# Kernel tuning notes

Measured on AMD Instinct MI355X. Metric: run time of the kernel, lower is better.

Reference implementation:

```python
import jax, jax.numpy as jnp
import numpy as np


def setup_inputs() -> dict:
    key0 = jax.random.key(0)
    ks = jax.random.split(key0, 6)
    b, q, k = 4, 256, 1024
    emb_q = emb_k = emb_v = 256
    h = 128
    query = jax.random.normal(ks[0], (b, q, emb_q), dtype=jnp.float32)
    key = jax.random.normal(ks[1], (b, k, emb_k), dtype=jnp.float32)
    value = jax.random.normal(ks[2], (b, k, emb_v), dtype=jnp.float32)
    # linear_uniform_ style init: U(-1/sqrt(in), 1/sqrt(in))
    wq = jax.random.uniform(ks[3], (emb_q, h), minval=-1.0, maxval=1.0) / np.sqrt(emb_q)
    wk = jax.random.uniform(ks[4], (emb_k, h), minval=-1.0, maxval=1.0) / np.sqrt(emb_k)
    wv = jax.random.uniform(ks[5], (h,), minval=-1.0, maxval=1.0) / np.sqrt(h)
    return {"query": query, "key": key, "value": value,
            "weight_query": wq.astype(jnp.float32),
            "weight_key": wk.astype(jnp.float32),
            "weight_value": wv.astype(jnp.float32)}


def reference(query, key, value, weight_query, weight_key, weight_value):
    # Additive (Bahdanau) attention.
    Hq = jnp.einsum('bqe,eh->bqh', query, weight_query)   # (b, q, h)
    Hk = jnp.einsum('bke,eh->bkh', key, weight_key)       # (b, k, h)
    # broadcast-add + tanh: (b, q, k, h)
    H = jnp.tanh(Hq[:, :, None, :] + Hk[:, None, :, :])
    z = jnp.einsum('bqkh,h->bqk', H, weight_value)        # scores (b, q, k)
    a = jax.nn.softmax(z, axis=-1)                        # (b, q, k)
    out = jnp.einsum('bqk,bkv->bqv', a, value)            # (b, q, emb_v)
    return out, a
```

## Files before the change

### kernel.cpp

```cpp
#include <hip/hip_runtime.h>


#define L2E 1.4426950408889634f

__global__ __launch_bounds__(256) void aa_proj_kernel(
    const float* __restrict__ query, const float* __restrict__ key,
    const float* __restrict__ wq, const float* __restrict__ wk,
    float* __restrict__ Eq, float* __restrict__ Ek)
{
    __shared__ float rows_s[16 * 256];
    __shared__ float w_s[64 * 128];
    const int i = blockIdx.x;
    const int t = threadIdx.x;

    const float* src;
    const float* W;
    float* dst;
    if (i < 64) {
        const int r0 = i * 16;
        src = query + r0 * 256; W = wq; dst = Eq + r0 * 128;
    } else {
        const int r0 = (i - 64) * 16;
        src = key + r0 * 256; W = wk; dst = Ek + r0 * 128;
    }

#pragma unroll
    for (int j = 0; j < 4; ++j) {
        const int f = t * 4 + j * 1024;
        *(float4*)&rows_s[f] = *(const float4*)&src[f];
    }

    const int rgr = t >> 5;
    const int hg = t & 31;
    const int ri0 = rgr * 2;
    const int h0 = hg * 4;

    float acc0[4] = {0.f, 0.f, 0.f, 0.f};
    float acc1[4] = {0.f, 0.f, 0.f, 0.f};

    for (int ec = 0; ec < 256; ec += 64) {
        __syncthreads();
#pragma unroll
        for (int j = 0; j < 8; ++j) {
            const int f = t * 4 + j * 1024;
            *(float4*)&w_s[f] = *(const float4*)&W[ec * 128 + f];
        }
        __syncthreads();

        for (int e = 0; e < 64; e += 4) {
            float a0[4], a1[4];
            *(float4*)a0 = *(const float4*)&rows_s[ri0 * 256 + ec + e];
            *(float4*)a1 = *(const float4*)&rows_s[(ri0 + 1) * 256 + ec + e];
#pragma unroll
            for (int j = 0; j < 4; ++j) {
                float w[4];
                *(float4*)w = *(const float4*)&w_s[(e + j) * 128 + h0];
#pragma unroll
                for (int c = 0; c < 4; ++c) {
                    acc0[c] = fmaf(a0[j], w[c], acc0[c]);
                    acc1[c] = fmaf(a1[j], w[c], acc1[c]);
                }
            }
        }
    }

    float o0[4], o1[4];
#pragma unroll
    for (int c = 0; c < 4; ++c) {
        o0[c] = __builtin_amdgcn_exp2f(acc0[c] * (2.0f * L2E));
        o1[c] = __builtin_amdgcn_exp2f(acc1[c] * (2.0f * L2E));
    }
    *(float4*)&dst[ri0 * 128 + h0] = *(float4*)o0;
    *(float4*)&dst[(ri0 + 1) * 128 + h0] = *(float4*)o1;
}

__global__ __launch_bounds__(256) void aa_score_kernel(
    const float* __restrict__ Eq, const float* __restrict__ Ek,
    const float* __restrict__ wv, float* __restrict__ z)
{
    __shared__ float eq_s[16 * 128];
    __shared__ float ek_s[64 * 132];
    __shared__ float wv_s[128];

    const int bid = blockIdx.x;
    const int b = bid >> 8;
    const int qt = (bid >> 4) & 15;
    const int kt = bid & 15;
    const int q0g = b * 256 + qt * 16;
    const int k0g = b * 1024 + kt * 64;
    const int t = threadIdx.x;

    const float* eqsrc = Eq + q0g * 128;
#pragma unroll
    for (int j = 0; j < 2; ++j) {
        const int f = t * 4 + j * 1024;
        *(float4*)&eq_s[f] = *(const float4*)&eqsrc[f];
    }
    const float* eksrc = Ek + k0g * 128;
#pragma unroll
    for (int j = 0; j < 8; ++j) {
        const int f = t * 4 + j * 1024;
        const int ki = f >> 7;
        const int h = f & 127;
        *(float4*)&ek_s[ki * 132 + h] = *(const float4*)&eksrc[f];
    }
    if (t < 128) wv_s[t] = wv[t];
    __syncthreads();

    float wsum = 0.f;
#pragma unroll
    for (int j = 0; j < 32; ++j) {
        float w4[4];
        *(float4*)w4 = *(const float4*)&wv_s[j * 4];
        wsum += (w4[0] + w4[1]) + (w4[2] + w4[3]);
    }

    const int qp = t >> 5;
    const int kp = t & 31;
    const float* eqa = eq_s + (qp * 2) * 128;
    const float* eqb = eqa + 128;
    const float* eka = ek_s + kp * 132;
    const float* ekb = eka + 32 * 132;

    float acc00 = 0.f, acc01 = 0.f, acc10 = 0.f, acc11 = 0.f;

    auto quad = [](const float* x, const float* y, const float* w, float& acc) {
        const float A = fmaf(x[0], y[0], 1.0f);
        const float B = fmaf(x[1], y[1], 1.0f);
        const float C = fmaf(x[2], y[2], 1.0f);
        const float D = fmaf(x[3], y[3], 1.0f);
        const float AB = A * B;
        const float CD = C * D;
        const float n01 = fmaf(w[1], A, w[0] * B);
        const float n23 = fmaf(w[3], C, w[2] * D);
        const float num = fmaf(n01, CD, n23 * AB);
        acc = fmaf(num, __builtin_amdgcn_rcpf(AB * CD), acc);
    };

#pragma unroll 4
    for (int h = 0; h < 128; h += 4) {
        float a0[4], a1[4], b0[4], b1[4], w[4];
        *(float4*)a0 = *(const float4*)(eqa + h);
        *(float4*)a1 = *(const float4*)(eqb + h);
        *(float4*)b0 = *(const float4*)(eka + h);
        *(float4*)b1 = *(const float4*)(ekb + h);
        *(float4*)w  = *(const float4*)(wv_s + h);
        quad(a0, b0, w, acc00);
        quad(a0, b1, w, acc01);
        quad(a1, b0, w, acc10);
        quad(a1, b1, w, acc11);
    }

    const int kl = kt * 64 + kp;
    float* zr0 = z + (size_t)(q0g + qp * 2) * 1024 + kl;
    float* zr1 = zr0 + 1024;
    zr0[0]  = fmaf(-2.f, acc00, wsum);
    zr0[32] = fmaf(-2.f, acc01, wsum);
    zr1[0]  = fmaf(-2.f, acc10, wsum);
    zr1[32] = fmaf(-2.f, acc11, wsum);
}

__global__ __launch_bounds__(256) void aa_softmax_kernel(
    const float* __restrict__ z, float* __restrict__ a)
{
    const int row = blockIdx.x;
    const int t = threadIdx.x;
    const float* zr = z + (size_t)row * 1024;

    float x[4];
    *(float4*)x = *(const float4*)&zr[t * 4];

    float m = fmaxf(fmaxf(x[0], x[1]), fmaxf(x[2], x[3]));
#pragma unroll
    for (int off = 32; off; off >>= 1) m = fmaxf(m, __shfl_xor(m, off));

    __shared__ float redm[4];
    __shared__ float reds[4];
    const int wid = t >> 6;
    if ((t & 63) == 0) redm[wid] = m;
    __syncthreads();
    m = fmaxf(fmaxf(redm[0], redm[1]), fmaxf(redm[2], redm[3]));

    float e[4];
    float s = 0.f;
#pragma unroll
    for (int j = 0; j < 4; ++j) {
        e[j] = __builtin_amdgcn_exp2f((x[j] - m) * L2E);
        s += e[j];
    }
#pragma unroll
    for (int off = 32; off; off >>= 1) s += __shfl_xor(s, off);
    if ((t & 63) == 0) reds[wid] = s;
    __syncthreads();
    s = reds[0] + reds[1] + reds[2] + reds[3];

    const float inv = __builtin_amdgcn_rcpf(s);
    float o[4];
#pragma unroll
    for (int j = 0; j < 4; ++j) o[j] = e[j] * inv;
    *(float4*)&a[(size_t)row * 1024 + t * 4] = *(float4*)o;
}

__global__ __launch_bounds__(256) void aa_pv_partial_kernel(
    const float* __restrict__ a, const float* __restrict__ value,
    float* __restrict__ part)
{
    __shared__ float a_s[16][128];
    __shared__ float red_s[4][4096];
    const int bid = blockIdx.x;
    const int b  = bid >> 7;
    const int qt = (bid >> 3) & 15;
    const int kt = bid & 7;
    const int t = threadIdx.x;

#pragma unroll
    for (int j = 0; j < 2; ++j) {
        const int f = t * 4 + j * 1024;
        const int qs = f >> 7;
        const int k0 = f & 127;
        const float* arow = a + (size_t)(b * 256 + qt * 16 + qs) * 1024 + kt * 128;
        *(float4*)&a_s[qs][k0] = *(const float4*)&arow[k0];
    }
    __syncthreads();

    const int w = t >> 6;
    const int lane = t & 63;
    const int v0 = lane * 4;
    const float* vp = value + (size_t)b * 262144
                    + (size_t)(kt * 128 + w * 32) * 256 + v0;

    float acc[16][4] = {};

#pragma unroll 2
    for (int k4 = 0; k4 < 8; ++k4) {
        float vv[4][4];
#pragma unroll
        for (int r = 0; r < 4; ++r)
            *(float4*)vv[r] = *(const float4*)(vp + (size_t)(k4 * 4 + r) * 256);
#pragma unroll
        for (int q = 0; q < 16; ++q) {
            float aq[4];
            *(float4*)aq = *(const float4*)&a_s[q][w * 32 + k4 * 4];
#pragma unroll
            for (int r = 0; r < 4; ++r)
#pragma unroll
                for (int c = 0; c < 4; ++c)
                    acc[q][c] = fmaf(aq[r], vv[r][c], acc[q][c]);
        }
    }

    float* rs = &red_s[w][v0];
#pragma unroll
    for (int q = 0; q < 16; ++q)
        *(float4*)(rs + q * 256) = *(float4*)acc[q];
    __syncthreads();

    const int g = t >> 6;
    const int l4 = (t & 63) * 4;
    float* po = part + (size_t)bid * 4096;
#pragma unroll
    for (int c = 0; c < 4; ++c) {
        const int i = g * 1024 + c * 256 + l4;
        float s[4];
        *(float4*)s = *(const float4*)&red_s[0][i];
#pragma unroll
        for (int ww = 1; ww < 4; ++ww) {
            float x[4];
            *(float4*)x = *(const float4*)&red_s[ww][i];
            s[0] += x[0]; s[1] += x[1]; s[2] += x[2]; s[3] += x[3];
        }
        *(float4*)(po + i) = *(float4*)s;
    }
}

__global__ __launch_bounds__(256) void aa_pv_reduce_kernel(
    const float* __restrict__ part, float* __restrict__ out)
{
    const int idx = blockIdx.x * 256 + threadIdx.x;
    const int o = idx * 4;
    const int row = o >> 8;
    const int v = o & 255;
    const int b = row >> 8;
    const int q = row & 255;
    const int qt = q >> 4;
    const int qr = q & 15;
    const float* p = part + (size_t)((b * 16 + qt) * 8) * 4096 + qr * 256 + v;

    float s[4] = {0.f, 0.f, 0.f, 0.f};
#pragma unroll
    for (int kt = 0; kt < 8; ++kt) {
        float x[4];
        *(float4*)x = *(const float4*)(p + (size_t)kt * 4096);
        s[0] += x[0]; s[1] += x[1]; s[2] += x[2]; s[3] += x[3];
    }
    *(float4*)&out[o] = *(float4*)s;
}

extern "C" void kernel_launch(void* const* d_in, const int* in_sizes, int n_in,
                              void* d_out, int out_size, void* d_ws, size_t ws_size,
                              hipStream_t stream)
{
    const float* query = (const float*)d_in[0];
    const float* key   = (const float*)d_in[1];
    const float* value = (const float*)d_in[2];
    const float* wq    = (const float*)d_in[3];
    const float* wk    = (const float*)d_in[4];
    const float* wv    = (const float*)d_in[5];

    float* out   = (float*)d_out;
    float* a_out = out + 4 * 256 * 256;

    float* ws = (float*)d_ws;
    float* Eq   = ws;
    float* Ek   = ws + 131072;
    float* z    = ws + 131072 + 524288;
    float* part = ws + 131072 + 524288 + 1048576;

    aa_proj_kernel<<<320, 256, 0, stream>>>(query, key, wq, wk, Eq, Ek);
    aa_score_kernel<<<1024, 256, 0, stream>>>(Eq, Ek, wv, z);
    aa_softmax_kernel<<<1024, 256, 0, stream>>>(z, a_out);
    aa_pv_partial_kernel<<<512, 256, 0, stream>>>(a_out, value, part);
    aa_pv_reduce_kernel<<<256, 256, 0, stream>>>(part, out);
}
```

Baseline: 53.47 us.

## Fuse score computation with row softmax, streaming key projections through LDS

Merges the score and softmax kernels into one. Each 512-thread block owns 4 query rows and streams the batch's 1024 projected keys through shared memory in 128-row chunks, prefetching the next chunk into registers. The full score row stays in registers, so the intermediate z buffer is never written or read back, and one launch disappears. The constant weight-sum term is dropped because softmax is shift-invariant. In exchange, each block re-reads the whole Ek for its batch, giving far more L2 traffic and less register reuse than the old 2x2 tiling, and the grid runs only one large block per CU.

Result: slower. 78.18 us (+46.2%).

```diff
diff --git a/kernel.cpp b/kernel.cpp
--- a/kernel.cpp
+++ b/kernel.cpp
@@ -74,131 +74,105 @@
     *(float4*)&dst[(ri0 + 1) * 128 + h0] = *(float4*)o1;
 }
 
-__global__ __launch_bounds__(256) void aa_score_kernel(
+__global__ __launch_bounds__(512) void aa_score_softmax_kernel(
     const float* __restrict__ Eq, const float* __restrict__ Ek,
-    const float* __restrict__ wv, float* __restrict__ z)
-{
-    __shared__ float eq_s[16 * 128];
-    __shared__ float ek_s[64 * 132];
-    __shared__ float wv_s[128];
+    const float* __restrict__ wv, float* __restrict__ a)
+{
+    __shared__ float ek_s[128 * 132];
 
     const int bid = blockIdx.x;
-    const int b = bid >> 8;
-    const int qt = (bid >> 4) & 15;
-    const int kt = bid & 15;
-    const int q0g = b * 256 + qt * 16;
-    const int k0g = b * 1024 + kt * 64;
-    const int t = threadIdx.x;
-
-    const float* eqsrc = Eq + q0g * 128;
-#pragma unroll
-    for (int j = 0; j < 2; ++j) {
-        const int f = t * 4 + j * 1024;
-        *(float4*)&eq_s[f] = *(const float4*)&eqsrc[f];
-    }
-    const float* eksrc = Ek + k0g * 128;
+    const int b  = bid >> 6;
+    const int qt = bid & 63;
+    const int t  = threadIdx.x;
+    const int qp = t >> 7;
+    const int kc = t & 127;
+    const int q0g = b * 256 + qt * 4;
+
+    const int qrow = __builtin_amdgcn_readfirstlane(q0g + qp);
+    const float* eqp = Eq + (size_t)qrow * 128;
+    const float* ekb = Ek + (size_t)b * 131072;
+
+    float pf[8][4];
 #pragma unroll
     for (int j = 0; j < 8; ++j) {
-        const int f = t * 4 + j * 1024;
-        const int ki = f >> 7;
-        const int h = f & 127;
-        *(float4*)&ek_s[ki * 132 + h] = *(const float4*)&eksrc[f];
-    }
-    if (t < 128) wv_s[t] = wv[t];
-    __syncthreads();
-
-    float wsum = 0.f;
-#pragma unroll
-    for (int j = 0; j < 32; ++j) {
-        float w4[4];
-        *(float4*)w4 = *(const float4*)&wv_s[j * 4];
-        wsum += (w4[0] + w4[1]) + (w4[2] + w4[3]);
-    }
-
-    const int qp = t >> 5;
-    const int kp = t & 31;
-    const float* eqa = eq_s + (qp * 2) * 128;
-    const float* eqb = eqa + 128;
-    const float* eka = ek_s + kp * 132;
-    const float* ekb = eka + 32 * 132;
-
-    float acc00 = 0.f, acc01 = 0.f, acc10 = 0.f, acc11 = 0.f;
-
-    auto quad = [](const float* x, const float* y, const float* w, float& acc) {
-        const float A = fmaf(x[0], y[0], 1.0f);
-        const float B = fmaf(x[1], y[1], 1.0f);
-        const float C = fmaf(x[2], y[2], 1.0f);
-        const float D = fmaf(x[3], y[3], 1.0f);
-        const float AB = A * B;
-        const float CD = C * D;
-        const float n01 = fmaf(w[1], A, w[0] * B);
-        const float n23 = fmaf(w[3], C, w[2] * D);
-        const float num = fmaf(n01, CD, n23 * AB);
-        acc = fmaf(num, __builtin_amdgcn_rcpf(AB * CD), acc);
-    };
-
-#pragma unroll 4
-    for (int h = 0; h < 128; h += 4) {
-        float a0[4], a1[4], b0[4], b1[4], w[4];
-        *(float4*)a0 = *(const float4*)(eqa + h);
-        *(float4*)a1 = *(const float4*)(eqb + h);
-        *(float4*)b0 = *(const float4*)(eka + h);
-        *(float4*)b1 = *(const float4*)(ekb + h);
-        *(float4*)w  = *(const float4*)(wv_s + h);
-        quad(a0, b0, w, acc00);
-        quad(a0, b1, w, acc01);
-        quad(a1, b0, w, acc10);
-        quad(a1, b1, w, acc11);
-    }
-
-    const int kl = kt * 64 + kp;
-    float* zr0 = z + (size_t)(q0g + qp * 2) * 1024 + kl;
-    float* zr1 = zr0 + 1024;
-    zr0[0]  = fmaf(-2.f, acc00, wsum);
-    zr0[32] = fmaf(-2.f, acc01, wsum);
-    zr1[0]  = fmaf(-2.f, acc10, wsum);
-    zr1[32] = fmaf(-2.f, acc11, wsum);
-}
-
-__global__ __launch_bounds__(256) void aa_softmax_kernel(
-    const float* __restrict__ z, float* __restrict__ a)
-{
-    const int row = blockIdx.x;
-    const int t = threadIdx.x;
-    const float* zr = z + (size_t)row * 1024;
-
-    float x[4];
-    *(float4*)x = *(const float4*)&zr[t * 4];
-
-    float m = fmaxf(fmaxf(x[0], x[1]), fmaxf(x[2], x[3]));
+        const int g = t * 4 + j * 2048;
+        *(float4*)pf[j] = *(const float4*)&ekb[g];
+    }
+
+    float zv[8];
+
+#pragma unroll
+    for (int c = 0; c < 8; ++c) {
+#pragma unroll
+        for (int j = 0; j < 8; ++j) {
+            const int g = t * 4 + j * 2048;
+            const int row = g >> 7;
+            const int col = g & 127;
+            *(float4*)&ek_s[row * 132 + col] = *(float4*)pf[j];
+        }
+        __syncthreads();
+
+        if (c < 7) {
+            const float* nx = ekb + (size_t)(c + 1) * 16384;
+#pragma unroll
+            for (int j = 0; j < 8; ++j) {
+                const int g = t * 4 + j * 2048;
+                *(float4*)pf[j] = *(const float4*)&nx[g];
+            }
+        }
+
+        float acc = 0.f;
+        const float* ekr = ek_s + kc * 132;
+#pragma unroll 8
+        for (int h = 0; h < 128; h += 4) {
+            float x[4], w4[4], y[4];
+            *(float4*)x  = *(const float4*)(eqp + h);
+            *(float4*)w4 = *(const float4*)(wv + h);
+            *(float4*)y  = *(const float4*)(ekr + h);
+            const float A = fmaf(x[0], y[0], 1.0f);
+            const float B = fmaf(x[1], y[1], 1.0f);
+            const float C = fmaf(x[2], y[2], 1.0f);
+            const float D = fmaf(x[3], y[3], 1.0f);
+            const float AB = A * B;
+            const float CD = C * D;
+            const float n01 = fmaf(w4[1], A, w4[0] * B);
+            const float n23 = fmaf(w4[3], C, w4[2] * D);
+            const float num = fmaf(n01, CD, n23 * AB);
+            acc = fmaf(num, __builtin_amdgcn_rcpf(AB * CD), acc);
+        }
+        zv[c] = -2.0f * acc;
+        __syncthreads();
+    }
+
+    float m = zv[0];
+#pragma unroll
+    for (int c = 1; c < 8; ++c) m = fmaxf(m, zv[c]);
 #pragma unroll
     for (int off = 32; off; off >>= 1) m = fmaxf(m, __shfl_xor(m, off));
 
-    __shared__ float redm[4];
-    __shared__ float reds[4];
-    const int wid = t >> 6;
-    if ((t & 63) == 0) redm[wid] = m;
-    __syncthreads();
-    m = fmaxf(fmaxf(redm[0], redm[1]), fmaxf(redm[2], redm[3]));
-
-    float e[4];
+    float* red = ek_s;
+    const int w = t >> 6;
+    if ((t & 63) == 0) red[w] = m;
+    __syncthreads();
+    m = fmaxf(red[qp * 2], red[qp * 2 + 1]);
+
+    float e[8];
     float s = 0.f;
 #pragma unroll
-    for (int j = 0; j < 4; ++j) {
-        e[j] = __builtin_amdgcn_exp2f((x[j] - m) * L2E);
-        s += e[j];
+    for (int c = 0; c < 8; ++c) {
+        e[c] = __builtin_amdgcn_exp2f((zv[c] - m) * L2E);
+        s += e[c];
     }
 #pragma unroll
     for (int off = 32; off; off >>= 1) s += __shfl_xor(s, off);
-    if ((t & 63) == 0) reds[wid] = s;
-    __syncthreads();
-    s = reds[0] + reds[1] + reds[2] + reds[3];
+    if ((t & 63) == 0) red[8 + w] = s;
+    __syncthreads();
+    s = red[8 + qp * 2] + red[8 + qp * 2 + 1];
 
     const float inv = __builtin_amdgcn_rcpf(s);
-    float o[4];
-#pragma unroll
-    for (int j = 0; j < 4; ++j) o[j] = e[j] * inv;
-    *(float4*)&a[(size_t)row * 1024 + t * 4] = *(float4*)o;
+    float* ar = a + (size_t)(q0g + qp) * 1024 + kc;
+#pragma unroll
+    for (int c = 0; c < 8; ++c) ar[c * 128] = e[c] * inv;
 }
 
 __global__ __launch_bounds__(256) void aa_pv_partial_kernel(
@@ -313,12 +287,10 @@
     float* ws = (float*)d_ws;
     float* Eq   = ws;
     float* Ek   = ws + 131072;
-    float* z    = ws + 131072 + 524288;
-    float* part = ws + 131072 + 524288 + 1048576;
+    float* part = ws + 131072 + 524288;
 
     aa_proj_kernel<<<320, 256, 0, stream>>>(query, key, wq, wk, Eq, Ek);
-    aa_score_kernel<<<1024, 256, 0, stream>>>(Eq, Ek, wv, z);
-    aa_softmax_kernel<<<1024, 256, 0, stream>>>(z, a_out);
+    aa_score_softmax_kernel<<<256, 512, 0, stream>>>(Eq, Ek, wv, a_out);
     aa_pv_partial_kernel<<<512, 256, 0, stream>>>(a_out, value, part);
     aa_pv_reduce_kernel<<<256, 256, 0, stream>>>(part, out);
 }
```

## Enlarge score and PV tiles, drop constant softmax offset

Applied to the files above, without the earlier changes.

The score kernel now covers 128 keys per block, with each thread computing 4 queries by 2 keys so each loaded key vector is reused more. It also drops the constant wsum term, which softmax shift-invariance makes redundant. The PV partial kernel uses 512 threads over 256-key tiles, halving the number of partials the reduce kernel must sum. The larger shared-memory footprints lower occupancy and give fewer blocks for latency hiding.

New measurement: 49.16 us. -8.1%, faster.

```diff
diff --git a/kernel.cpp b/kernel.cpp
--- a/kernel.cpp
+++ b/kernel.cpp
@@ -79,26 +79,26 @@
     const float* __restrict__ wv, float* __restrict__ z)
 {
     __shared__ float eq_s[16 * 128];
-    __shared__ float ek_s[64 * 132];
+    __shared__ float ek_s[128 * 132];
     __shared__ float wv_s[128];
 
     const int bid = blockIdx.x;
-    const int b = bid >> 8;
-    const int qt = (bid >> 4) & 15;
-    const int kt = bid & 15;
+    const int b  = bid >> 7;
+    const int qt = (bid >> 3) & 15;
+    const int kt = bid & 7;
     const int q0g = b * 256 + qt * 16;
-    const int k0g = b * 1024 + kt * 64;
+    const int k0g = b * 1024 + kt * 128;
     const int t = threadIdx.x;
 
-    const float* eqsrc = Eq + q0g * 128;
+    const float* eqsrc = Eq + (size_t)q0g * 128;
 #pragma unroll
     for (int j = 0; j < 2; ++j) {
         const int f = t * 4 + j * 1024;
         *(float4*)&eq_s[f] = *(const float4*)&eqsrc[f];
     }
-    const float* eksrc = Ek + k0g * 128;
-#pragma unroll
-    for (int j = 0; j < 8; ++j) {
+    const float* eksrc = Ek + (size_t)k0g * 128;
+#pragma unroll
+    for (int j = 0; j < 16; ++j) {
         const int f = t * 4 + j * 1024;
         const int ki = f >> 7;
         const int h = f & 127;
@@ -107,22 +107,13 @@
     if (t < 128) wv_s[t] = wv[t];
     __syncthreads();
 
-    float wsum = 0.f;
-#pragma unroll
-    for (int j = 0; j < 32; ++j) {
-        float w4[4];
-        *(float4*)w4 = *(const float4*)&wv_s[j * 4];
-        wsum += (w4[0] + w4[1]) + (w4[2] + w4[3]);
-    }
-
-    const int qp = t >> 5;
-    const int kp = t & 31;
-    const float* eqa = eq_s + (qp * 2) * 128;
-    const float* eqb = eqa + 128;
+    const int qp = t >> 6;
+    const int kp = t & 63;
+    const float* eq0 = eq_s + (qp * 4) * 128;
     const float* eka = ek_s + kp * 132;
-    const float* ekb = eka + 32 * 132;
-
-    float acc00 = 0.f, acc01 = 0.f, acc10 = 0.f, acc11 = 0.f;
+    const float* ekb = eka + 64 * 132;
+
+    float acc[4][2] = {};
 
     auto quad = [](const float* x, const float* y, const float* w, float& acc) {
         const float A = fmaf(x[0], y[0], 1.0f);
@@ -139,25 +130,26 @@
 
 #pragma unroll 4
     for (int h = 0; h < 128; h += 4) {
-        float a0[4], a1[4], b0[4], b1[4], w[4];
-        *(float4*)a0 = *(const float4*)(eqa + h);
-        *(float4*)a1 = *(const float4*)(eqb + h);
-        *(float4*)b0 = *(const float4*)(eka + h);
-        *(float4*)b1 = *(const float4*)(ekb + h);
-        *(float4*)w  = *(const float4*)(wv_s + h);
-        quad(a0, b0, w, acc00);
-        quad(a0, b1, w, acc01);
-        quad(a1, b0, w, acc10);
-        quad(a1, b1, w, acc11);
-    }
-
-    const int kl = kt * 64 + kp;
-    float* zr0 = z + (size_t)(q0g + qp * 2) * 1024 + kl;
-    float* zr1 = zr0 + 1024;
-    zr0[0]  = fmaf(-2.f, acc00, wsum);
-    zr0[32] = fmaf(-2.f, acc01, wsum);
-    zr1[0]  = fmaf(-2.f, acc10, wsum);
-    zr1[32] = fmaf(-2.f, acc11, wsum);
+        float y0[4], y1[4], w4[4];
+        *(float4*)y0 = *(const float4*)(eka + h);
+        *(float4*)y1 = *(const float4*)(ekb + h);
+        *(float4*)w4 = *(const float4*)(wv_s + h);
+#pragma unroll
+        for (int i = 0; i < 4; ++i) {
+            float x[4];
+            *(float4*)x = *(const float4*)(eq0 + i * 128 + h);
+            quad(x, y0, w4, acc[i][0]);
+            quad(x, y1, w4, acc[i][1]);
+        }
+    }
+
+    const int kl = kt * 128 + kp;
+#pragma unroll
+    for (int i = 0; i < 4; ++i) {
+        float* zr = z + (size_t)(q0g + qp * 4 + i) * 1024 + kl;
+        zr[0]  = -2.0f * acc[i][0];
+        zr[64] = -2.0f * acc[i][1];
+    }
 }
 
 __global__ __launch_bounds__(256) void aa_softmax_kernel(
@@ -201,24 +193,24 @@
     *(float4*)&a[(size_t)row * 1024 + t * 4] = *(float4*)o;
 }
 
-__global__ __launch_bounds__(256) void aa_pv_partial_kernel(
+__global__ __launch_bounds__(512) void aa_pv_partial_kernel(
     const float* __restrict__ a, const float* __restrict__ value,
     float* __restrict__ part)
 {
-    __shared__ float a_s[16][128];
-    __shared__ float red_s[4][4096];
+    __shared__ float a_s[16][256];
+    __shared__ float red_s[8][4096];
     const int bid = blockIdx.x;
-    const int b  = bid >> 7;
-    const int qt = (bid >> 3) & 15;
-    const int kt = bid & 7;
+    const int b  = bid >> 6;
+    const int qt = (bid >> 2) & 15;
+    const int kt = bid & 3;
     const int t = threadIdx.x;
 
 #pragma unroll
     for (int j = 0; j < 2; ++j) {
-        const int f = t * 4 + j * 1024;
-        const int qs = f >> 7;
-        const int k0 = f & 127;
-        const float* arow = a + (size_t)(b * 256 + qt * 16 + qs) * 1024 + kt * 128;
+        const int f = t * 4 + j * 2048;
+        const int qs = f >> 8;
+        const int k0 = f & 255;
+        const float* arow = a + (size_t)(b * 256 + qt * 16 + qs) * 1024 + kt * 256;
         *(float4*)&a_s[qs][k0] = *(const float4*)&arow[k0];
     }
     __syncthreads();
@@ -227,7 +219,7 @@
     const int lane = t & 63;
     const int v0 = lane * 4;
     const float* vp = value + (size_t)b * 262144
-                    + (size_t)(kt * 128 + w * 32) * 256 + v0;
+                    + (size_t)(kt * 256 + w * 32) * 256 + v0;
 
     float acc[16][4] = {};
 
@@ -255,16 +247,14 @@
         *(float4*)(rs + q * 256) = *(float4*)acc[q];
     __syncthreads();
 
-    const int g = t >> 6;
-    const int l4 = (t & 63) * 4;
     float* po = part + (size_t)bid * 4096;
 #pragma unroll
-    for (int c = 0; c < 4; ++c) {
-        const int i = g * 1024 + c * 256 + l4;
+    for (int c = 0; c < 2; ++c) {
+        const int i = c * 2048 + t * 4;
         float s[4];
         *(float4*)s = *(const float4*)&red_s[0][i];
 #pragma unroll
-        for (int ww = 1; ww < 4; ++ww) {
+        for (int ww = 1; ww < 8; ++ww) {
             float x[4];
             *(float4*)x = *(const float4*)&red_s[ww][i];
             s[0] += x[0]; s[1] += x[1]; s[2] += x[2]; s[3] += x[3];
@@ -284,11 +274,11 @@
     const int q = row & 255;
     const int qt = q >> 4;
     const int qr = q & 15;
-    const float* p = part + (size_t)((b * 16 + qt) * 8) * 4096 + qr * 256 + v;
+    const float* p = part + (size_t)((b * 16 + qt) * 4) * 4096 + qr * 256 + v;
 
     float s[4] = {0.f, 0.f, 0.f, 0.f};
 #pragma unroll
-    for (int kt = 0; kt < 8; ++kt) {
+    for (int kt = 0; kt < 4; ++kt) {
         float x[4];
         *(float4*)x = *(const float4*)(p + (size_t)kt * 4096);
         s[0] += x[0]; s[1] += x[1]; s[2] += x[2]; s[3] += x[3];
@@ -317,8 +307,8 @@
     float* part = ws + 131072 + 524288 + 1048576;
 
     aa_proj_kernel<<<320, 256, 0, stream>>>(query, key, wq, wk, Eq, Ek);
-    aa_score_kernel<<<1024, 256, 0, stream>>>(Eq, Ek, wv, z);
+    aa_score_kernel<<<512, 256, 0, stream>>>(Eq, Ek, wv, z);
     aa_softmax_kernel<<<1024, 256, 0, stream>>>(z, a_out);
-    aa_pv_partial_kernel<<<512, 256, 0, stream>>>(a_out, value, part);
+    aa_pv_partial_kernel<<<256, 512, 0, stream>>>(a_out, value, part);
     aa_pv_reduce_kernel<<<256, 256, 0, stream>>>(part, out);
 }
```
